# Kernel optimization log

Hardware: AMD Instinct MI355X
Metric: run time of the kernel (lower is better)

## Reference

```python
import jax, jax.numpy as jnp
import numpy as np

TNEI = 2
TOPK = 4
NEIGH = 2 * TNEI + 1  # window size = 5


def _normalize(x, eps=1e-12):
    # matches torch F.normalize(dim=-1)
    n = jnp.linalg.norm(x, axis=-1, keepdims=True)
    return x / jnp.maximum(n, eps)


def setup_inputs() -> dict:
    key = jax.random.key(0)
    ks = jax.random.split(key, 10)
    B, T, C = 32, 256, 128
    x = jax.random.normal(ks[0], (B, T, C), jnp.float32)
    radj = jax.random.randint(ks[1], (B, T, T), 0, 2).astype(jnp.int32)
    inxs = jax.random.randint(ks[2], (B, T, TOPK), 0, T)
    s = 1.0 / np.sqrt(C)
    W_pf = jax.random.normal(ks[3], (C, C), jnp.float32) * s
    W_ns = jax.random.normal(ks[4], (C, C), jnp.float32) * s
    W_v = jax.random.normal(ks[5], (C, C), jnp.float32) * s
    v_pf = jax.random.normal(ks[6], (NEIGH,), jnp.float32)
    g_pf = jnp.linalg.norm(v_pf)[None]  # weight_norm gain, shape (1,)
    v_ns = jax.random.normal(ks[7], (TOPK,), jnp.float32)
    g_ns = jnp.linalg.norm(v_ns)[None]
    return dict(x=x, radj=radj, inxs=inxs, W_pf=W_pf, W_ns=W_ns, W_v=W_v,
                v_pf=v_pf, g_pf=g_pf, v_ns=v_ns, g_ns=g_ns)


def reference(x, radj, inxs, W_pf, W_ns, W_v, v_pf, g_pf, v_ns, g_ns):
    B, T, C = x.shape
    pf = _normalize(x @ W_pf.T)
    ns = _normalize(x @ W_ns.T)
    v = x @ W_v.T
    # windowed neighbor indices, identical to _tneigh_mask(mode='all')
    i = jnp.arange(T)
    start = jnp.clip(i - TNEI, 0, T - NEIGH)
    nbr = start[:, None] + jnp.arange(NEIGH)[None, :]  # (T, NEIGH)
    ctx = pf[:, nbr]  # (B, T, NEIGH, C) — replaces one-hot ctxinx einsum
    # pairwise window similarity: (B,T,T,n,n)
    sim = jnp.einsum('bxic,byjc->bxyij', ctx, ctx)
    # AdaptiveMaxPool2d((n,1)) == max over the last (key-window) axis
    sim_pf = sim.max(axis=-1)  # (B,T,T,n)
    w_pf = g_pf[0] * v_pf / jnp.linalg.norm(v_pf)  # weight-norm agg_pf
    sim_pf = jnp.einsum('bxyi,i->bxy', sim_pf, w_pf)
    # topk-neighbor branch: inxs gathers ns rows (replaces one-hot einsum)
    ns_q = ns[jnp.arange(B)[:, None, None], inxs]  # (B,T,TOPK,C)
    sim_ns = jnp.einsum('bxnc,byc->bxyn', ns_q, ns)  # (B,T,T,TOPK)
    w_ns = g_ns[0] * v_ns / jnp.linalg.norm(v_ns)  # weight-norm agg_ns
    sim_ns = jnp.einsum('bxyn,n->bxy', sim_ns, w_ns)
    # adjacency mask: 0 -> -1e22, >0 -> 0
    mask = jnp.where(radj == 0, jnp.float32(-1e22), jnp.float32(0.0))
    attn = jax.nn.softmax(sim_pf + sim_ns + mask, axis=-1)  # (B,T,T)
    return jnp.einsum('bkt,btd->bkd', attn, v)  # (B,T,C)
```

## Files before the change

### kernel.cpp

```cpp
#include <hip/hip_runtime.h>
#include <math.h>


#define TT 256
#define CC 128

using bf16x8 = __attribute__((ext_vector_type(8))) short;
using f32x4  = __attribute__((ext_vector_type(4))) float;

__device__ __forceinline__ short bf_hi(float x) {
    unsigned u = __float_as_uint(x);
    return (short)((u + 0x7FFFu + ((u >> 16) & 1u)) >> 16);
}
__device__ __forceinline__ void bf_split(float x, short& h, short& l) {
    h = bf_hi(x);
    float hf = __uint_as_float(((unsigned)(unsigned short)h) << 16);
    l = bf_hi(x - hf);
}

__global__ __launch_bounds__(256) void proj_kernel(
    const float* __restrict__ x,
    const float* __restrict__ W0, const float* __restrict__ W1, const float* __restrict__ W2,
    float* __restrict__ o0, float* __restrict__ o1, float* __restrict__ o2)
{
    __shared__ float xs[64][36];
    __shared__ float Ws[128][36];
    const int tid = threadIdx.x, ty = tid >> 4, tx = tid & 15;
    const int row0 = blockIdx.x * 64;
    const int m = blockIdx.y;
    const float* __restrict__ W = (m == 0) ? W0 : (m == 1) ? W1 : W2;
    float* __restrict__ o = (m == 0) ? o0 : (m == 1) ? o1 : o2;
    float acc[4][8] = {};

    for (int k0 = 0; k0 < CC; k0 += 32) {
        __syncthreads();
        for (int i = 0; i < 2; i++) {
            int flat = i * 256 + tid, r = flat >> 3, q = (flat & 7) * 4;
            *(float4*)&xs[r][q] = *(const float4*)&x[(row0 + r) * CC + k0 + q];
        }
        for (int i = 0; i < 4; i++) {
            int flat = i * 256 + tid, r = flat >> 3, q = (flat & 7) * 4;
            *(float4*)&Ws[r][q] = *(const float4*)&W[r * CC + k0 + q];
        }
        __syncthreads();
        for (int kq = 0; kq < 32; kq += 4) {
            float4 av[4], bv[8];
            for (int u = 0; u < 4; u++) av[u] = *(float4*)&xs[ty + 16 * u][kq];
            for (int w = 0; w < 8; w++) bv[w] = *(float4*)&Ws[tx + 16 * w][kq];
            for (int u = 0; u < 4; u++)
                for (int w = 0; w < 8; w++) {
                    acc[u][w] = fmaf(av[u].x, bv[w].x, acc[u][w]);
                    acc[u][w] = fmaf(av[u].y, bv[w].y, acc[u][w]);
                    acc[u][w] = fmaf(av[u].z, bv[w].z, acc[u][w]);
                    acc[u][w] = fmaf(av[u].w, bv[w].w, acc[u][w]);
                }
        }
    }
    for (int u = 0; u < 4; u++) {
        float inv = 1.f;
        if (m < 2) {
            float ss = 0.f;
            for (int w = 0; w < 8; w++) ss += acc[u][w] * acc[u][w];
            for (int off = 8; off; off >>= 1) ss += __shfl_xor(ss, off);
            inv = 1.f / fmaxf(sqrtf(ss), 1e-12f);
        }
        int row = row0 + ty + 16 * u;
        for (int w = 0; w < 8; w++)
            o[row * CC + tx + 16 * w] = acc[u][w] * inv;
    }
}

__global__ __launch_bounds__(256, 4) void gram_mfma(
    const float* __restrict__ pf, const float* __restrict__ ns,
    const int* __restrict__ inxs, const float* __restrict__ v_ns,
    const float* __restrict__ g_ns, float* __restrict__ G, float* __restrict__ S)
{
    __shared__ short Ah[64 * 40], Al[64 * 40], Bh[64 * 40], Bl[64 * 40];
    const int tid = threadIdx.x;
    const int m0 = blockIdx.x * 64, n0 = blockIdx.y * 64;
    const int b = blockIdx.z >> 1, half = blockIdx.z & 1;
    const float* __restrict__ Pb = pf + b * TT * CC;
    const float* __restrict__ Nb = ns + b * TT * CC;
    const float* __restrict__ Bsrc = half ? Nb : Pb;

    float w0 = 0.f, w1 = 0.f, w2 = 0.f, w3 = 0.f;
    int4 id0 = {0, 0, 0, 0}, id1 = {0, 0, 0, 0};
    if (half) {
        float n2 = v_ns[0]*v_ns[0] + v_ns[1]*v_ns[1] + v_ns[2]*v_ns[2] + v_ns[3]*v_ns[3];
        float sc = g_ns[0] / sqrtf(n2);
        w0 = sc*v_ns[0]; w1 = sc*v_ns[1]; w2 = sc*v_ns[2]; w3 = sc*v_ns[3];
        id0 = *(const int4*)&inxs[(b * TT + m0 + (tid >> 3)) * 4];
        id1 = *(const int4*)&inxs[(b * TT + m0 + 32 + (tid >> 3)) * 4];
    }

    const int lane = tid & 63, wave = tid >> 6;
    const int wm = wave >> 1, wn = wave & 1;
    const int quad = lane >> 4, lr = lane & 15;
    f32x4 z4 = {0.f, 0.f, 0.f, 0.f};
    f32x4 acc[2][2] = {{z4, z4}, {z4, z4}};

    for (int k0 = 0; k0 < CC; k0 += 32) {
        __syncthreads();
        for (int i = 0; i < 2; i++) {
            int flat = i * 256 + tid, r = flat >> 3, q = (flat & 7) * 4;
            float4 a4;
            if (!half) {
                a4 = *(const float4*)&Pb[(m0 + r) * CC + k0 + q];
            } else {
                int4 id = i ? id1 : id0;
                float4 aa = *(const float4*)&Nb[id.x * CC + k0 + q];
                float4 ab = *(const float4*)&Nb[id.y * CC + k0 + q];
                float4 ac = *(const float4*)&Nb[id.z * CC + k0 + q];
                float4 ad = *(const float4*)&Nb[id.w * CC + k0 + q];
                a4.x = w0*aa.x + w1*ab.x + w2*ac.x + w3*ad.x;
                a4.y = w0*aa.y + w1*ab.y + w2*ac.y + w3*ad.y;
                a4.z = w0*aa.z + w1*ab.z + w2*ac.z + w3*ad.z;
                a4.w = w0*aa.w + w1*ab.w + w2*ac.w + w3*ad.w;
            }
            float4 b4 = *(const float4*)&Bsrc[(n0 + r) * CC + k0 + q];
            short4 h4, l4;
            bf_split(a4.x, h4.x, l4.x); bf_split(a4.y, h4.y, l4.y);
            bf_split(a4.z, h4.z, l4.z); bf_split(a4.w, h4.w, l4.w);
            *(short4*)&Ah[r * 40 + q] = h4; *(short4*)&Al[r * 40 + q] = l4;
            bf_split(b4.x, h4.x, l4.x); bf_split(b4.y, h4.y, l4.y);
            bf_split(b4.z, h4.z, l4.z); bf_split(b4.w, h4.w, l4.w);
            *(short4*)&Bh[r * 40 + q] = h4; *(short4*)&Bl[r * 40 + q] = l4;
        }
        __syncthreads();
        bf16x8 bh[2], bl[2];
        for (int tn = 0; tn < 2; tn++) {
            int br = (32 * wn + 16 * tn + lr) * 40 + quad * 8;
            bh[tn] = *(bf16x8*)&Bh[br];
            bl[tn] = *(bf16x8*)&Bl[br];
        }
        for (int tm = 0; tm < 2; tm++) {
            int ar = (32 * wm + 16 * tm + lr) * 40 + quad * 8;
            bf16x8 ah = *(bf16x8*)&Ah[ar];
            bf16x8 al = *(bf16x8*)&Al[ar];
            for (int tn = 0; tn < 2; tn++) {
                acc[tm][tn] = __builtin_amdgcn_mfma_f32_16x16x32_bf16(ah, bh[tn], acc[tm][tn], 0, 0, 0);
                acc[tm][tn] = __builtin_amdgcn_mfma_f32_16x16x32_bf16(ah, bl[tn], acc[tm][tn], 0, 0, 0);
                acc[tm][tn] = __builtin_amdgcn_mfma_f32_16x16x32_bf16(al, bh[tn], acc[tm][tn], 0, 0, 0);
            }
        }
    }
    float* __restrict__ Cb = (half ? S : G) + b * TT * TT;
    for (int tm = 0; tm < 2; tm++)
        for (int tn = 0; tn < 2; tn++) {
            int rb = m0 + 32 * wm + 16 * tm + quad * 4;
            int cb = n0 + 32 * wn + 16 * tn + lr;
            for (int reg = 0; reg < 4; reg++)
                Cb[(rb + reg) * TT + cb] = acc[tm][tn][reg];
        }
}

#define GS_ 0
#define RM_ 5120
#define AT_ 10320
#define RD_ 14480
#define RMX_ 14544
#define VS_ 0
#define PP_ 4224
__global__ __launch_bounds__(256, 2) void fused_smax_pv(
    const float* __restrict__ G, const float* __restrict__ S,
    const int* __restrict__ radj, const float* __restrict__ v_pf,
    const float* __restrict__ g_pf, const float* __restrict__ V,
    float* __restrict__ out)
{
    __shared__ float lds[14608];
    const int tid = threadIdx.x;
    const int xt = blockIdx.x, b = blockIdx.y;
    const int x0 = xt * 16;
    const int rbase = min(max(x0 - 2, 0), TT - 5);
    for (int i = 0; i < 5; i++) {
        int flat = i * 256 + tid, ri = flat >> 6, q = (flat & 63) * 4;
        int r = min(rbase + ri, TT - 1);
        *(float4*)&lds[GS_ + ri * 256 + q] = *(const float4*)&G[b * TT * TT + r * TT + q];
    }
    float n2 = 0.f;
    for (int i = 0; i < 5; i++) n2 += v_pf[i] * v_pf[i];
    float sc = g_pf[0] / sqrtf(n2);
    float wpf[5];
    for (int i = 0; i < 5; i++) wpf[i] = sc * v_pf[i];
    __syncthreads();

    const int y = tid;
    const int sy = min(max(y - 2, 0), TT - 5);
    for (int i = 0; i < 20; i++) {
        const float* row = &lds[GS_ + i * 256 + sy];
        float mx = row[0];
        for (int j = 1; j < 5; j++) mx = fmaxf(mx, row[j]);
        lds[RM_ + i * 260 + y] = mx;
    }
    float lv[16];
    for (int xi = 0; xi < 16; xi++) {
        int sxr = min(max(x0 + xi - 2, 0), TT - 5) - rbase;
        float s = 0.f;
        for (int i = 0; i < 5; i++)
            s = fmaf(wpf[i], lds[RM_ + (sxr + i) * 260 + y], s);
        s += S[b * TT * TT + (x0 + xi) * TT + y];
        if (radj[(b * TT + x0 + xi) * TT + y] == 0) s += -1e22f;
        lv[xi] = s;
    }
    const int lane = tid & 63, wv = tid >> 6;
    for (int xi = 0; xi < 16; xi++) {
        float v = lv[xi];
        for (int o = 32; o; o >>= 1) v = fmaxf(v, __shfl_xor(v, o));
        if (lane == 0) lds[RMX_ + xi * 4 + wv] = v;
    }
    __syncthreads();
    for (int xi = 0; xi < 16; xi++) {
        float mx = fmaxf(fmaxf(lds[RMX_ + xi * 4], lds[RMX_ + xi * 4 + 1]),
                         fmaxf(lds[RMX_ + xi * 4 + 2], lds[RMX_ + xi * 4 + 3]));
        float e = __expf(lv[xi] - mx);
        lds[AT_ + xi * 260 + y] = e;
        for (int o = 32; o; o >>= 1) e += __shfl_xor(e, o);
        if (lane == 0) lds[RD_ + xi * 4 + wv] = e;
    }
    const int tx = tid & 15, qt = (tid >> 4) & 3, w = tid >> 6;
    const float* __restrict__ Vb = V + b * TT * CC;
    float4 a0[4] = {}, a1[4] = {};
    for (int c = 0; c < 8; c++) {
        int kk0 = c * 32;
        __syncthreads();
        for (int i = 0; i < 4; i++) {
            int flat = i * 256 + tid, kk = flat >> 5, q = (flat & 31) * 4;
            *(float4*)&lds[VS_ + kk * 132 + q] = *(const float4*)&Vb[(kk0 + kk) * CC + q];
        }
        __syncthreads();
        for (int s = 0; s < 2; s++) {
            int kl = w * 8 + s * 4;
            float atv[4][4];
            for (int j = 0; j < 4; j++) {
                float4 t = *(float4*)&lds[AT_ + (qt * 4 + j) * 260 + kk0 + kl];
                atv[j][0] = t.x; atv[j][1] = t.y; atv[j][2] = t.z; atv[j][3] = t.w;
            }
            for (int kk = 0; kk < 4; kk++) {
                float4 v0 = *(float4*)&lds[VS_ + (kl + kk) * 132 + 8 * tx];
                float4 v1 = *(float4*)&lds[VS_ + (kl + kk) * 132 + 8 * tx + 4];
                for (int j = 0; j < 4; j++) {
                    float a = atv[j][kk];
                    a0[j].x = fmaf(a, v0.x, a0[j].x); a0[j].y = fmaf(a, v0.y, a0[j].y);
                    a0[j].z = fmaf(a, v0.z, a0[j].z); a0[j].w = fmaf(a, v0.w, a0[j].w);
                    a1[j].x = fmaf(a, v1.x, a1[j].x); a1[j].y = fmaf(a, v1.y, a1[j].y);
                    a1[j].z = fmaf(a, v1.z, a1[j].z); a1[j].w = fmaf(a, v1.w, a1[j].w);
                }
            }
        }
    }
    __syncthreads();
    for (int j = 0; j < 4; j++) {
        *(float4*)&lds[PP_ + (w * 16 + qt * 4 + j) * 128 + 8 * tx]     = a0[j];
        *(float4*)&lds[PP_ + (w * 16 + qt * 4 + j) * 128 + 8 * tx + 4] = a1[j];
    }
    __syncthreads();
    const int q = tid >> 4, c0 = (tid & 15) * 8;
    float4 r0 = {0, 0, 0, 0}, r1 = {0, 0, 0, 0};
    for (int ww = 0; ww < 4; ww++) {
        float4 p0 = *(float4*)&lds[PP_ + (ww * 16 + q) * 128 + c0];
        float4 p1 = *(float4*)&lds[PP_ + (ww * 16 + q) * 128 + c0 + 4];
        r0.x += p0.x; r0.y += p0.y; r0.z += p0.z; r0.w += p0.w;
        r1.x += p1.x; r1.y += p1.y; r1.z += p1.z; r1.w += p1.w;
    }
    float sm = lds[RD_ + q * 4] + lds[RD_ + q * 4 + 1] + lds[RD_ + q * 4 + 2] + lds[RD_ + q * 4 + 3];
    float rinv = 1.f / sm;
    r0.x *= rinv; r0.y *= rinv; r0.z *= rinv; r0.w *= rinv;
    r1.x *= rinv; r1.y *= rinv; r1.z *= rinv; r1.w *= rinv;
    *(float4*)&out[b * TT * CC + (x0 + q) * CC + c0]     = r0;
    *(float4*)&out[b * TT * CC + (x0 + q) * CC + c0 + 4] = r1;
}

extern "C" void kernel_launch(void* const* d_in, const int* in_sizes, int n_in,
                              void* d_out, int out_size, void* d_ws, size_t ws_size,
                              hipStream_t stream) {
    const float* x    = (const float*)d_in[0];
    const int*   radj = (const int*)d_in[1];
    const int*   inxs = (const int*)d_in[2];
    const float* Wpf  = (const float*)d_in[3];
    const float* Wns  = (const float*)d_in[4];
    const float* Wv   = (const float*)d_in[5];
    const float* v_pf = (const float*)d_in[6];
    const float* g_pf = (const float*)d_in[7];
    const float* v_ns = (const float*)d_in[8];
    const float* g_ns = (const float*)d_in[9];
    float* out = (float*)d_out;

    float* ws = (float*)d_ws;
    float* pf = ws;
    float* ns = ws + (1u << 20);
    float* vv = ws + 2u * (1u << 20);
    float* G  = ws + 4u * (1u << 20);
    float* S  = ws + 6u * (1u << 20);

    proj_kernel<<<dim3(128, 3), 256, 0, stream>>>(x, Wpf, Wns, Wv, pf, ns, vv);
    gram_mfma<<<dim3(4, 4, 64), 256, 0, stream>>>(pf, ns, inxs, v_ns, g_ns, G, S);
    fused_smax_pv<<<dim3(16, 32), 256, 0, stream>>>(G, S, radj, v_pf, g_pf, vv, out);
}
```

Measured before the change: 129.8 us.

## Presplit operands to bf16 hi/lo, add prep kernel, use MFMA for attn·V

The projection kernel now writes pf and ns already split into bf16 hi/lo halves. A new prep kernel builds the weighted top-k query rows and a transposed, split copy of V. The gram kernel drops its LDS staging and reads the pre-split fragments straight from global memory. The softmax kernel replaces its scalar FMA attention-times-V loop with 3-pass bf16 MFMA and computes the window max with vectorised neighbour loads. This removes repeated split and gather work and the scalar PV cost, at the price of an extra launch and more workspace traffic.

```diff
diff --git a/kernel.cpp b/kernel.cpp
--- a/kernel.cpp
+++ b/kernel.cpp
@@ -17,11 +17,16 @@
     float hf = __uint_as_float(((unsigned)(unsigned short)h) << 16);
     l = bf_hi(x - hf);
 }
+__device__ __forceinline__ float max5(float a, float b, float c, float d, float e) {
+    return fmaxf(fmaxf(fmaxf(a, b), fmaxf(c, d)), e);
+}
 
 __global__ __launch_bounds__(256) void proj_kernel(
     const float* __restrict__ x,
     const float* __restrict__ W0, const float* __restrict__ W1, const float* __restrict__ W2,
-    float* __restrict__ o0, float* __restrict__ o1, float* __restrict__ o2)
+    short* __restrict__ pf_h, short* __restrict__ pf_l,
+    short* __restrict__ ns_h, short* __restrict__ ns_l,
+    float* __restrict__ ns_f, float* __restrict__ v_f)
 {
     __shared__ float xs[64][36];
     __shared__ float Ws[128][36];
@@ -29,7 +34,6 @@
     const int row0 = blockIdx.x * 64;
     const int m = blockIdx.y;
     const float* __restrict__ W = (m == 0) ? W0 : (m == 1) ? W1 : W2;
-    float* __restrict__ o = (m == 0) ? o0 : (m == 1) ? o1 : o2;
     float acc[4][8] = {};
 
     for (int k0 = 0; k0 < CC; k0 += 32) {
@@ -57,117 +61,151 @@
         }
     }
     for (int u = 0; u < 4; u++) {
-        float inv = 1.f;
-        if (m < 2) {
+        int row = row0 + ty + 16 * u;
+        if (m == 2) {
+            for (int w = 0; w < 8; w++) v_f[row * CC + tx + 16 * w] = acc[u][w];
+        } else {
             float ss = 0.f;
             for (int w = 0; w < 8; w++) ss += acc[u][w] * acc[u][w];
             for (int off = 8; off; off >>= 1) ss += __shfl_xor(ss, off);
-            inv = 1.f / fmaxf(sqrtf(ss), 1e-12f);
-        }
-        int row = row0 + ty + 16 * u;
-        for (int w = 0; w < 8; w++)
-            o[row * CC + tx + 16 * w] = acc[u][w] * inv;
-    }
-}
-
-__global__ __launch_bounds__(256, 4) void gram_mfma(
-    const float* __restrict__ pf, const float* __restrict__ ns,
-    const int* __restrict__ inxs, const float* __restrict__ v_ns,
-    const float* __restrict__ g_ns, float* __restrict__ G, float* __restrict__ S)
+            float inv = 1.f / fmaxf(sqrtf(ss), 1e-12f);
+            for (int w = 0; w < 8; w++) {
+                float v = acc[u][w] * inv;
+                short h, l;
+                bf_split(v, h, l);
+                int idx = row * CC + tx + 16 * w;
+                if (m == 0) { pf_h[idx] = h; pf_l[idx] = l; }
+                else        { ns_h[idx] = h; ns_l[idx] = l; ns_f[idx] = v; }
+            }
+        }
+    }
+}
+
+__global__ __launch_bounds__(256) void prep_kernel(
+    const float* __restrict__ ns_f, const int* __restrict__ inxs,
+    const float* __restrict__ v_ns, const float* __restrict__ g_ns,
+    const float* __restrict__ v_f,
+    short* __restrict__ q_h, short* __restrict__ q_l,
+    short* __restrict__ vt_h, short* __restrict__ vt_l)
 {
-    __shared__ short Ah[64 * 40], Al[64 * 40], Bh[64 * 40], Bl[64 * 40];
+    __shared__ float Ls[64][132];
+    const int bx = blockIdx.x, tid = threadIdx.x;
+    if (bx < 512) {
+        float n2 = v_ns[0]*v_ns[0] + v_ns[1]*v_ns[1] + v_ns[2]*v_ns[2] + v_ns[3]*v_ns[3];
+        float sc = g_ns[0] / sqrtf(n2);
+        const float w0 = sc*v_ns[0], w1 = sc*v_ns[1], w2 = sc*v_ns[2], w3 = sc*v_ns[3];
+        for (int it = 0; it < 2; it++) {
+            int t4 = bx * 512 + it * 256 + tid;
+            int q = (t4 & 31) * 4, gr = t4 >> 5;
+            int b = gr >> 8;
+            int4 id = *(const int4*)&inxs[gr * 4];
+            const float* Nb = ns_f + (size_t)b * TT * CC;
+            float4 aa = *(const float4*)&Nb[id.x * CC + q];
+            float4 ab = *(const float4*)&Nb[id.y * CC + q];
+            float4 ac = *(const float4*)&Nb[id.z * CC + q];
+            float4 ad = *(const float4*)&Nb[id.w * CC + q];
+            float4 r4;
+            r4.x = w0*aa.x + w1*ab.x + w2*ac.x + w3*ad.x;
+            r4.y = w0*aa.y + w1*ab.y + w2*ac.y + w3*ad.y;
+            r4.z = w0*aa.z + w1*ab.z + w2*ac.z + w3*ad.z;
+            r4.w = w0*aa.w + w1*ab.w + w2*ac.w + w3*ad.w;
+            short4 h4, l4;
+            bf_split(r4.x, h4.x, l4.x); bf_split(r4.y, h4.y, l4.y);
+            bf_split(r4.z, h4.z, l4.z); bf_split(r4.w, h4.w, l4.w);
+            *(short4*)&q_h[(size_t)gr * CC + q] = h4;
+            *(short4*)&q_l[(size_t)gr * CC + q] = l4;
+        }
+    } else {
+        int blk = bx - 512;
+        int b = blk >> 2, t0 = (blk & 3) * 64;
+        const float* Vb = v_f + (size_t)b * TT * CC;
+        for (int i = 0; i < 8; i++) {
+            int flat = i * 256 + tid, r = flat >> 5, cq = (flat & 31) * 4;
+            *(float4*)&Ls[r][cq] = *(const float4*)&Vb[(t0 + r) * CC + cq];
+        }
+        __syncthreads();
+        int c = tid & 127, th = tid >> 7;
+        for (int j = 0; j < 8; j++) {
+            short4 h4, l4;
+            for (int e = 0; e < 4; e++) {
+                float v = Ls[th * 32 + j * 4 + e][c];
+                bf_split(v, ((short*)&h4)[e], ((short*)&l4)[e]);
+            }
+            size_t o = ((size_t)b * CC + c) * TT + t0 + th * 32 + j * 4;
+            *(short4*)&vt_h[o] = h4;
+            *(short4*)&vt_l[o] = l4;
+        }
+    }
+}
+
+__global__ __launch_bounds__(256) void gram_mfma(
+    const short* __restrict__ pf_h, const short* __restrict__ pf_l,
+    const short* __restrict__ ns_h, const short* __restrict__ ns_l,
+    const short* __restrict__ q_h,  const short* __restrict__ q_l,
+    float* __restrict__ G, float* __restrict__ S)
+{
     const int tid = threadIdx.x;
     const int m0 = blockIdx.x * 64, n0 = blockIdx.y * 64;
     const int b = blockIdx.z >> 1, half = blockIdx.z & 1;
-    const float* __restrict__ Pb = pf + b * TT * CC;
-    const float* __restrict__ Nb = ns + b * TT * CC;
-    const float* __restrict__ Bsrc = half ? Nb : Pb;
-
-    float w0 = 0.f, w1 = 0.f, w2 = 0.f, w3 = 0.f;
-    int4 id0 = {0, 0, 0, 0}, id1 = {0, 0, 0, 0};
-    if (half) {
-        float n2 = v_ns[0]*v_ns[0] + v_ns[1]*v_ns[1] + v_ns[2]*v_ns[2] + v_ns[3]*v_ns[3];
-        float sc = g_ns[0] / sqrtf(n2);
-        w0 = sc*v_ns[0]; w1 = sc*v_ns[1]; w2 = sc*v_ns[2]; w3 = sc*v_ns[3];
-        id0 = *(const int4*)&inxs[(b * TT + m0 + (tid >> 3)) * 4];
-        id1 = *(const int4*)&inxs[(b * TT + m0 + 32 + (tid >> 3)) * 4];
-    }
-
+    const size_t base = (size_t)b * TT * CC;
+    const short* __restrict__ Ahp = (half ? q_h : pf_h) + base;
+    const short* __restrict__ Alp = (half ? q_l : pf_l) + base;
+    const short* __restrict__ Bhp = (half ? ns_h : pf_h) + base;
+    const short* __restrict__ Blp = (half ? ns_l : pf_l) + base;
     const int lane = tid & 63, wave = tid >> 6;
     const int wm = wave >> 1, wn = wave & 1;
     const int quad = lane >> 4, lr = lane & 15;
+    const int am0 = (m0 + 32 * wm + lr) * CC, am1 = am0 + 16 * CC;
+    const int bn0 = (n0 + 32 * wn + lr) * CC, bn1 = bn0 + 16 * CC;
     f32x4 z4 = {0.f, 0.f, 0.f, 0.f};
     f32x4 acc[2][2] = {{z4, z4}, {z4, z4}};
-
+    #pragma unroll
     for (int k0 = 0; k0 < CC; k0 += 32) {
-        __syncthreads();
-        for (int i = 0; i < 2; i++) {
-            int flat = i * 256 + tid, r = flat >> 3, q = (flat & 7) * 4;
-            float4 a4;
-            if (!half) {
-                a4 = *(const float4*)&Pb[(m0 + r) * CC + k0 + q];
-            } else {
-                int4 id = i ? id1 : id0;
-                float4 aa = *(const float4*)&Nb[id.x * CC + k0 + q];
-                float4 ab = *(const float4*)&Nb[id.y * CC + k0 + q];
-                float4 ac = *(const float4*)&Nb[id.z * CC + k0 + q];
-                float4 ad = *(const float4*)&Nb[id.w * CC + k0 + q];
-                a4.x = w0*aa.x + w1*ab.x + w2*ac.x + w3*ad.x;
-                a4.y = w0*aa.y + w1*ab.y + w2*ac.y + w3*ad.y;
-                a4.z = w0*aa.z + w1*ab.z + w2*ac.z + w3*ad.z;
-                a4.w = w0*aa.w + w1*ab.w + w2*ac.w + w3*ad.w;
-            }
-            float4 b4 = *(const float4*)&Bsrc[(n0 + r) * CC + k0 + q];
-            short4 h4, l4;
-            bf_split(a4.x, h4.x, l4.x); bf_split(a4.y, h4.y, l4.y);
-            bf_split(a4.z, h4.z, l4.z); bf_split(a4.w, h4.w, l4.w);
-            *(short4*)&Ah[r * 40 + q] = h4; *(short4*)&Al[r * 40 + q] = l4;
-            bf_split(b4.x, h4.x, l4.x); bf_split(b4.y, h4.y, l4.y);
-            bf_split(b4.z, h4.z, l4.z); bf_split(b4.w, h4.w, l4.w);
-            *(short4*)&Bh[r * 40 + q] = h4; *(short4*)&Bl[r * 40 + q] = l4;
-        }
-        __syncthreads();
-        bf16x8 bh[2], bl[2];
-        for (int tn = 0; tn < 2; tn++) {
-            int br = (32 * wn + 16 * tn + lr) * 40 + quad * 8;
-            bh[tn] = *(bf16x8*)&Bh[br];
-            bl[tn] = *(bf16x8*)&Bl[br];
-        }
-        for (int tm = 0; tm < 2; tm++) {
-            int ar = (32 * wm + 16 * tm + lr) * 40 + quad * 8;
-            bf16x8 ah = *(bf16x8*)&Ah[ar];
-            bf16x8 al = *(bf16x8*)&Al[ar];
-            for (int tn = 0; tn < 2; tn++) {
-                acc[tm][tn] = __builtin_amdgcn_mfma_f32_16x16x32_bf16(ah, bh[tn], acc[tm][tn], 0, 0, 0);
-                acc[tm][tn] = __builtin_amdgcn_mfma_f32_16x16x32_bf16(ah, bl[tn], acc[tm][tn], 0, 0, 0);
-                acc[tm][tn] = __builtin_amdgcn_mfma_f32_16x16x32_bf16(al, bh[tn], acc[tm][tn], 0, 0, 0);
-            }
-        }
-    }
-    float* __restrict__ Cb = (half ? S : G) + b * TT * TT;
+        int ko = k0 + quad * 8;
+        bf16x8 a0h = *(const bf16x8*)&Ahp[am0 + ko];
+        bf16x8 a0l = *(const bf16x8*)&Alp[am0 + ko];
+        bf16x8 a1h = *(const bf16x8*)&Ahp[am1 + ko];
+        bf16x8 a1l = *(const bf16x8*)&Alp[am1 + ko];
+        bf16x8 b0h = *(const bf16x8*)&Bhp[bn0 + ko];
+        bf16x8 b0l = *(const bf16x8*)&Blp[bn0 + ko];
+        bf16x8 b1h = *(const bf16x8*)&Bhp[bn1 + ko];
+        bf16x8 b1l = *(const bf16x8*)&Blp[bn1 + ko];
+        acc[0][0] = __builtin_amdgcn_mfma_f32_16x16x32_bf16(a0h, b0h, acc[0][0], 0, 0, 0);
+        acc[0][0] = __builtin_amdgcn_mfma_f32_16x16x32_bf16(a0h, b0l, acc[0][0], 0, 0, 0);
+        acc[0][0] = __builtin_amdgcn_mfma_f32_16x16x32_bf16(a0l, b0h, acc[0][0], 0, 0, 0);
+        acc[0][1] = __builtin_amdgcn_mfma_f32_16x16x32_bf16(a0h, b1h, acc[0][1], 0, 0, 0);
+        acc[0][1] = __builtin_amdgcn_mfma_f32_16x16x32_bf16(a0h, b1l, acc[0][1], 0, 0, 0);
+        acc[0][1] = __builtin_amdgcn_mfma_f32_16x16x32_bf16(a0l, b1h, acc[0][1], 0, 0, 0);
+        acc[1][0] = __builtin_amdgcn_mfma_f32_16x16x32_bf16(a1h, b0h, acc[1][0], 0, 0, 0);
+        acc[1][0] = __builtin_amdgcn_mfma_f32_16x16x32_bf16(a1h, b0l, acc[1][0], 0, 0, 0);
+        acc[1][0] = __builtin_amdgcn_mfma_f32_16x16x32_bf16(a1l, b0h, acc[1][0], 0, 0, 0);
+        acc[1][1] = __builtin_amdgcn_mfma_f32_16x16x32_bf16(a1h, b1h, acc[1][1], 0, 0, 0);
+        acc[1][1] = __builtin_amdgcn_mfma_f32_16x16x32_bf16(a1h, b1l, acc[1][1], 0, 0, 0);
+        acc[1][1] = __builtin_amdgcn_mfma_f32_16x16x32_bf16(a1l, b1h, acc[1][1], 0, 0, 0);
+    }
+    float* __restrict__ Cb = (half ? S : G) + (size_t)b * TT * TT;
     for (int tm = 0; tm < 2; tm++)
         for (int tn = 0; tn < 2; tn++) {
             int rb = m0 + 32 * wm + 16 * tm + quad * 4;
             int cb = n0 + 32 * wn + 16 * tn + lr;
             for (int reg = 0; reg < 4; reg++)
-                Cb[(rb + reg) * TT + cb] = acc[tm][tn][reg];
-        }
-}
-
-#define GS_ 0
-#define RM_ 5120
-#define AT_ 10320
-#define RD_ 14480
-#define RMX_ 14544
-#define VS_ 0
-#define PP_ 4224
+                Cb[(size_t)(rb + reg) * TT + cb] = acc[tm][tn][reg];
+        }
+}
+
 __global__ __launch_bounds__(256, 2) void fused_smax_pv(
     const float* __restrict__ G, const float* __restrict__ S,
     const int* __restrict__ radj, const float* __restrict__ v_pf,
-    const float* __restrict__ g_pf, const float* __restrict__ V,
+    const float* __restrict__ g_pf,
+    const short* __restrict__ vt_h, const short* __restrict__ vt_l,
     float* __restrict__ out)
 {
-    __shared__ float lds[14608];
+    __shared__ float Gs[20 * 256];
+    __shared__ float RM[20 * 256];
+    __shared__ short ATH[16 * 264];
+    __shared__ short ATL[16 * 264];
+    __shared__ float RD[64];
+    __shared__ float RMX[64];
     const int tid = threadIdx.x;
     const int xt = blockIdx.x, b = blockIdx.y;
     const int x0 = xt * 16;
@@ -175,7 +213,7 @@
     for (int i = 0; i < 5; i++) {
         int flat = i * 256 + tid, ri = flat >> 6, q = (flat & 63) * 4;
         int r = min(rbase + ri, TT - 1);
-        *(float4*)&lds[GS_ + ri * 256 + q] = *(const float4*)&G[b * TT * TT + r * TT + q];
+        *(float4*)&Gs[ri * 256 + q] = *(const float4*)&G[(size_t)b * TT * TT + r * TT + q];
     }
     float n2 = 0.f;
     for (int i = 0; i < 5; i++) n2 += v_pf[i] * v_pf[i];
@@ -183,91 +221,110 @@
     float wpf[5];
     for (int i = 0; i < 5; i++) wpf[i] = sc * v_pf[i];
     __syncthreads();
-
+    for (int t = 0; t < 5; t++) {
+        int task = t * 256 + tid;
+        int i = task >> 6, g = task & 63;
+        const float* row = &Gs[i * 256];
+        float4 X = *(float4*)&row[4 * g];
+        float m0_, m1_, m2_, m3_;
+        if (g == 0) {
+            float4 N = *(float4*)&row[4];
+            float mx = fmaxf(fmaxf(X.x, X.y), fmaxf(X.z, X.w));
+            m0_ = m1_ = m2_ = fmaxf(mx, N.x);
+            m3_ = max5(X.y, X.z, X.w, N.x, N.y);
+        } else if (g == 63) {
+            float4 P = *(float4*)&row[248];
+            m0_ = max5(P.z, P.w, X.x, X.y, X.z);
+            float mx = fmaxf(fmaxf(X.x, X.y), fmaxf(X.z, X.w));
+            m1_ = m2_ = m3_ = fmaxf(P.w, mx);
+        } else {
+            float4 P = *(float4*)&row[4 * g - 4];
+            float4 N = *(float4*)&row[4 * g + 4];
+            m0_ = max5(P.z, P.w, X.x, X.y, X.z);
+            m1_ = max5(P.w, X.x, X.y, X.z, X.w);
+            m2_ = max5(X.x, X.y, X.z, X.w, N.x);
+            m3_ = max5(X.y, X.z, X.w, N.x, N.y);
+        }
+        float4 o4 = {m0_, m1_, m2_, m3_};
+        *(float4*)&RM[i * 256 + 4 * g] = o4;
+    }
+    __syncthreads();
     const int y = tid;
-    const int sy = min(max(y - 2, 0), TT - 5);
-    for (int i = 0; i < 20; i++) {
-        const float* row = &lds[GS_ + i * 256 + sy];
-        float mx = row[0];
-        for (int j = 1; j < 5; j++) mx = fmaxf(mx, row[j]);
-        lds[RM_ + i * 260 + y] = mx;
-    }
+    const size_t sb = (size_t)b * TT * TT;
     float lv[16];
+    if (xt > 0 && xt < 15) {
+        float rm[20];
+        #pragma unroll
+        for (int r = 0; r < 20; r++) rm[r] = RM[r * 256 + y];
+        #pragma unroll
+        for (int xi = 0; xi < 16; xi++) {
+            float s = wpf[0] * rm[xi];
+            #pragma unroll
+            for (int i = 1; i < 5; i++) s = fmaf(wpf[i], rm[xi + i], s);
+            lv[xi] = s;
+        }
+    } else {
+        for (int xi = 0; xi < 16; xi++) {
+            int sxr = min(max(x0 + xi - 2, 0), TT - 5) - rbase;
+            float s = 0.f;
+            for (int i = 0; i < 5; i++) s = fmaf(wpf[i], RM[(sxr + i) * 256 + y], s);
+            lv[xi] = s;
+        }
+    }
     for (int xi = 0; xi < 16; xi++) {
-        int sxr = min(max(x0 + xi - 2, 0), TT - 5) - rbase;
-        float s = 0.f;
-        for (int i = 0; i < 5; i++)
-            s = fmaf(wpf[i], lds[RM_ + (sxr + i) * 260 + y], s);
-        s += S[b * TT * TT + (x0 + xi) * TT + y];
-        if (radj[(b * TT + x0 + xi) * TT + y] == 0) s += -1e22f;
-        lv[xi] = s;
+        lv[xi] += S[sb + (x0 + xi) * TT + y];
+        if (radj[sb + (x0 + xi) * TT + y] == 0) lv[xi] += -1e22f;
     }
     const int lane = tid & 63, wv = tid >> 6;
     for (int xi = 0; xi < 16; xi++) {
         float v = lv[xi];
         for (int o = 32; o; o >>= 1) v = fmaxf(v, __shfl_xor(v, o));
-        if (lane == 0) lds[RMX_ + xi * 4 + wv] = v;
+        if (lane == 0) RMX[xi * 4 + wv] = v;
     }
     __syncthreads();
     for (int xi = 0; xi < 16; xi++) {
-        float mx = fmaxf(fmaxf(lds[RMX_ + xi * 4], lds[RMX_ + xi * 4 + 1]),
-                         fmaxf(lds[RMX_ + xi * 4 + 2], lds[RMX_ + xi * 4 + 3]));
+        float mx = fmaxf(fmaxf(RMX[xi * 4], RMX[xi * 4 + 1]),
+                         fmaxf(RMX[xi * 4 + 2], RMX[xi * 4 + 3]));
         float e = __expf(lv[xi] - mx);
-        lds[AT_ + xi * 260 + y] = e;
+        short h, l;
+        bf_split(e, h, l);
+        ATH[xi * 264 + y] = h;
+        ATL[xi * 264 + y] = l;
         for (int o = 32; o; o >>= 1) e += __shfl_xor(e, o);
-        if (lane == 0) lds[RD_ + xi * 4 + wv] = e;
-    }
-    const int tx = tid & 15, qt = (tid >> 4) & 3, w = tid >> 6;
-    const float* __restrict__ Vb = V + b * TT * CC;
-    float4 a0[4] = {}, a1[4] = {};
-    for (int c = 0; c < 8; c++) {
-        int kk0 = c * 32;
-        __syncthreads();
-        for (int i = 0; i < 4; i++) {
-            int flat = i * 256 + tid, kk = flat >> 5, q = (flat & 31) * 4;
-            *(float4*)&lds[VS_ + kk * 132 + q] = *(const float4*)&Vb[(kk0 + kk) * CC + q];
-        }
-        __syncthreads();
-        for (int s = 0; s < 2; s++) {
-            int kl = w * 8 + s * 4;
-            float atv[4][4];
-            for (int j = 0; j < 4; j++) {
-                float4 t = *(float4*)&lds[AT_ + (qt * 4 + j) * 260 + kk0 + kl];
-                atv[j][0] = t.x; atv[j][1] = t.y; atv[j][2] = t.z; atv[j][3] = t.w;
-            }
-            for (int kk = 0; kk < 4; kk++) {
-                float4 v0 = *(float4*)&lds[VS_ + (kl + kk) * 132 + 8 * tx];
-                float4 v1 = *(float4*)&lds[VS_ + (kl + kk) * 132 + 8 * tx + 4];
-                for (int j = 0; j < 4; j++) {
-                    float a = atv[j][kk];
-                    a0[j].x = fmaf(a, v0.x, a0[j].x); a0[j].y = fmaf(a, v0.y, a0[j].y);
-                    a0[j].z = fmaf(a, v0.z, a0[j].z); a0[j].w = fmaf(a, v0.w, a0[j].w);
-                    a1[j].x = fmaf(a, v1.x, a1[j].x); a1[j].y = fmaf(a, v1.y, a1[j].y);
-                    a1[j].z = fmaf(a, v1.z, a1[j].z); a1[j].w = fmaf(a, v1.w, a1[j].w);
-                }
-            }
-        }
+        if (lane == 0) RD[xi * 4 + wv] = e;
     }
     __syncthreads();
-    for (int j = 0; j < 4; j++) {
-        *(float4*)&lds[PP_ + (w * 16 + qt * 4 + j) * 128 + 8 * tx]     = a0[j];
-        *(float4*)&lds[PP_ + (w * 16 + qt * 4 + j) * 128 + 8 * tx + 4] = a1[j];
-    }
-    __syncthreads();
-    const int q = tid >> 4, c0 = (tid & 15) * 8;
-    float4 r0 = {0, 0, 0, 0}, r1 = {0, 0, 0, 0};
-    for (int ww = 0; ww < 4; ww++) {
-        float4 p0 = *(float4*)&lds[PP_ + (ww * 16 + q) * 128 + c0];
-        float4 p1 = *(float4*)&lds[PP_ + (ww * 16 + q) * 128 + c0 + 4];
-        r0.x += p0.x; r0.y += p0.y; r0.z += p0.z; r0.w += p0.w;
-        r1.x += p1.x; r1.y += p1.y; r1.z += p1.z; r1.w += p1.w;
-    }
-    float sm = lds[RD_ + q * 4] + lds[RD_ + q * 4 + 1] + lds[RD_ + q * 4 + 2] + lds[RD_ + q * 4 + 3];
+    const int quad = lane >> 4, lr = lane & 15;
+    const int c0 = wv * 32;
+    const short* __restrict__ vhb = vt_h + (size_t)b * CC * TT;
+    const short* __restrict__ vlb = vt_l + (size_t)b * CC * TT;
+    const int ar0 = (c0 + lr) * TT, ar1 = ar0 + 16 * TT;
+    f32x4 z4 = {0.f, 0.f, 0.f, 0.f};
+    f32x4 acc[2] = {z4, z4};
+    #pragma unroll
+    for (int k0 = 0; k0 < TT; k0 += 32) {
+        int ko = k0 + quad * 8;
+        bf16x8 bh = *(bf16x8*)&ATH[lr * 264 + ko];
+        bf16x8 bl = *(bf16x8*)&ATL[lr * 264 + ko];
+        bf16x8 a0h = *(const bf16x8*)&vhb[ar0 + ko];
+        bf16x8 a0l = *(const bf16x8*)&vlb[ar0 + ko];
+        bf16x8 a1h = *(const bf16x8*)&vhb[ar1 + ko];
+        bf16x8 a1l = *(const bf16x8*)&vlb[ar1 + ko];
+        acc[0] = __builtin_amdgcn_mfma_f32_16x16x32_bf16(a0h, bh, acc[0], 0, 0, 0);
+        acc[0] = __builtin_amdgcn_mfma_f32_16x16x32_bf16(a0h, bl, acc[0], 0, 0, 0);
+        acc[0] = __builtin_amdgcn_mfma_f32_16x16x32_bf16(a0l, bh, acc[0], 0, 0, 0);
+        acc[1] = __builtin_amdgcn_mfma_f32_16x16x32_bf16(a1h, bh, acc[1], 0, 0, 0);
+        acc[1] = __builtin_amdgcn_mfma_f32_16x16x32_bf16(a1h, bl, acc[1], 0, 0, 0);
+        acc[1] = __builtin_amdgcn_mfma_f32_16x16x32_bf16(a1l, bh, acc[1], 0, 0, 0);
+    }
+    float sm = RD[lr * 4] + RD[lr * 4 + 1] + RD[lr * 4 + 2] + RD[lr * 4 + 3];
     float rinv = 1.f / sm;
-    r0.x *= rinv; r0.y *= rinv; r0.z *= rinv; r0.w *= rinv;
-    r1.x *= rinv; r1.y *= rinv; r1.z *= rinv; r1.w *= rinv;
-    *(float4*)&out[b * TT * CC + (x0 + q) * CC + c0]     = r0;
-    *(float4*)&out[b * TT * CC + (x0 + q) * CC + c0 + 4] = r1;
+    for (int tm = 0; tm < 2; tm++) {
+        float4 r;
+        r.x = acc[tm][0] * rinv; r.y = acc[tm][1] * rinv;
+        r.z = acc[tm][2] * rinv; r.w = acc[tm][3] * rinv;
+        *(float4*)&out[(size_t)b * TT * CC + (x0 + lr) * CC + c0 + 16 * tm + quad * 4] = r;
+    }
 }
 
 extern "C" void kernel_launch(void* const* d_in, const int* in_sizes, int n_in,
@@ -285,14 +342,25 @@
     const float* g_ns = (const float*)d_in[9];
     float* out = (float*)d_out;
 
-    float* ws = (float*)d_ws;
-    float* pf = ws;
-    float* ns = ws + (1u << 20);
-    float* vv = ws + 2u * (1u << 20);
-    float* G  = ws + 4u * (1u << 20);
-    float* S  = ws + 6u * (1u << 20);
-
-    proj_kernel<<<dim3(128, 3), 256, 0, stream>>>(x, Wpf, Wns, Wv, pf, ns, vv);
-    gram_mfma<<<dim3(4, 4, 64), 256, 0, stream>>>(pf, ns, inxs, v_ns, g_ns, G, S);
-    fused_smax_pv<<<dim3(16, 32), 256, 0, stream>>>(G, S, radj, v_pf, g_pf, vv, out);
-}
+    char* base = (char*)d_ws;
+    float* ns_f = (float*)(base);
+    float* v_f  = (float*)(base + (4u << 20));
+    short* pf_h = (short*)(base + (8u << 20));
+    short* pf_l = (short*)(base + (10u << 20));
+    short* ns_h = (short*)(base + (12u << 20));
+    short* ns_l = (short*)(base + (14u << 20));
+    short* q_h  = (short*)(base + (16u << 20));
+    short* q_l  = (short*)(base + (18u << 20));
+    short* vt_h = (short*)(base + (20u << 20));
+    short* vt_l = (short*)(base + (22u << 20));
+    float* G    = (float*)(base + (24u << 20));
+    float* S    = (float*)(base + (32u << 20));
+
+    proj_kernel<<<dim3(128, 3), 256, 0, stream>>>(x, Wpf, Wns, Wv,
+                                                  pf_h, pf_l, ns_h, ns_l, ns_f, v_f);
+    prep_kernel<<<640, 256, 0, stream>>>(ns_f, inxs, v_ns, g_ns, v_f,
+                                         q_h, q_l, vt_h, vt_l);
+    gram_mfma<<<dim3(4, 4, 64), 256, 0, stream>>>(pf_h, pf_l, ns_h, ns_l, q_h, q_l, G, S);
+    fused_smax_pv<<<dim3(16, 32), 256, 0, stream>>>(G, S, radj, v_pf, g_pf,
+                                                    vt_h, vt_l, out);
+}
```

Result: slower. 144.5 us (+11.4%).
